# Kernel optimization log

Measured on AMD Instinct MI355X. Metric: run time of the kernel, lower is better.

Reference implementation:

```python
import jax, jax.numpy as jnp
import numpy as np

B, S, HID = 2, 2048, 1024
NUM_HEADS, HEAD_DIM = 16, 64
GRID_SIZE = 16                 # crop_size // patch_size
ROT_DIM = 2 * (HEAD_DIM // 3 // 2)  # = 20, per axial segment (d, h, w)


def setup_inputs() -> dict:
    key = jax.random.key(0)
    ks = jax.random.split(key, 9)
    sc = 1.0 / np.sqrt(HID)
    return {
        "hidden_states": jax.random.normal(ks[0], (B, S, HID), jnp.float32),
        "Wq": jax.random.normal(ks[1], (HID, HID), jnp.float32) * sc,
        "bq": jax.random.normal(ks[2], (HID,), jnp.float32) * 0.02,
        "Wk": jax.random.normal(ks[3], (HID, HID), jnp.float32) * sc,
        "bk": jax.random.normal(ks[4], (HID,), jnp.float32) * 0.02,
        "Wv": jax.random.normal(ks[5], (HID, HID), jnp.float32) * sc,
        "bv": jax.random.normal(ks[6], (HID,), jnp.float32) * 0.02,
        "Wo": jax.random.normal(ks[7], (HID, HID), jnp.float32) * sc,
        "bo": jax.random.normal(ks[8], (HID,), jnp.float32) * 0.02,
    }


def _rotate(x, pos):
    # x: [B, H, S, D], pos: [S] int. Matches torch rotate_queries_or_keys:
    # sin/cos are TILED (repeat) along the last dim, not interleaved.
    D = x.shape[-1]
    half = D // 2
    omega = 1.0 / (10000.0 ** (jnp.arange(half, dtype=x.dtype) / half))
    freq = pos.astype(x.dtype)[:, None] * omega           # [S, half]
    sin = jnp.tile(jnp.sin(freq), (1, 2))                 # [S, D]
    cos = jnp.tile(jnp.cos(freq), (1, 2))
    y = x.reshape(x.shape[:-1] + (half, 2))
    rot = jnp.stack((-y[..., 1], y[..., 0]), axis=-1).reshape(x.shape)
    return x * cos + rot * sin


def _apply_axial_rope(qk, frame_ids, height_ids, width_ids):
    d = ROT_DIM
    parts = [
        _rotate(qk[..., 0:d], frame_ids),
        _rotate(qk[..., d:2 * d], height_ids),
        _rotate(qk[..., 2 * d:3 * d], width_ids),
    ]
    if 3 * d < qk.shape[-1]:
        parts.append(qk[..., 3 * d:])  # un-rotated tail
    return jnp.concatenate(parts, axis=-1)


def reference(hidden_states, Wq, bq, Wk, bk, Wv, bv, Wo, bo):
    Bq, Sq, _ = hidden_states.shape

    def heads(x):  # [B,S,HID] -> [B,H,S,Dh]
        return x.reshape(Bq, Sq, NUM_HEADS, HEAD_DIM).transpose(0, 2, 1, 3)

    q = heads(hidden_states @ Wq + bq)
    k = heads(hidden_states @ Wk + bk)
    v = heads(hidden_states @ Wv + bv)

    # 3D axial position ids from flat token index
    ids = jnp.arange(Sq)
    tokens_per_frame = GRID_SIZE * GRID_SIZE
    frame_ids = ids // tokens_per_frame
    rem = ids - tokens_per_frame * frame_ids
    height_ids = rem // GRID_SIZE
    width_ids = rem - GRID_SIZE * height_ids

    k = _apply_axial_rope(k, frame_ids, height_ids, width_ids)
    q = _apply_axial_rope(q, frame_ids, height_ids, width_ids)

    scaling = HEAD_DIM ** -0.5
    scores = jnp.einsum("bhqd,bhkd->bhqk", q, k) * scaling
    probs = jax.nn.softmax(scores.astype(jnp.float32), axis=-1).astype(q.dtype)
    ctx = jnp.einsum("bhqk,bhkd->bhqd", probs, v)
    ctx = ctx.transpose(0, 2, 1, 3).reshape(Bq, Sq, HID)
    return ctx @ Wo + bo
```

## Files before the change

### kernel.cpp

```cpp
#include <hip/hip_runtime.h>
#include <hip/hip_bf16.h>

#define B_   2
#define S_   2048
#define HID_ 1024
#define NH_  16
#define HD_  64

typedef __hip_bfloat16 bf16;
typedef __attribute__((ext_vector_type(8))) short s8v;
typedef __attribute__((ext_vector_type(4))) float f4v;

#define QSCALE 0.18033688011112042f

__device__ __forceinline__ unsigned short f2b_rne(float x) {
    unsigned int u = __float_as_uint(x);
    u += 0x7fffu + ((u >> 16) & 1u);
    return (unsigned short)(u >> 16);
}

__device__ __forceinline__ void gload_lds16(const void* g, void* l) {
    __builtin_amdgcn_global_load_lds(
        (const __attribute__((address_space(1))) void*)g,
        (__attribute__((address_space(3))) void*)l, 16, 0, 0);
}

__global__ __launch_bounds__(256) void convert_x_kernel(
    const float* __restrict__ X, unsigned short* __restrict__ Xb)
{
    const int i = (blockIdx.x * 256 + threadIdx.x) * 4;
    const float4 f = *reinterpret_cast<const float4*>(X + i);
    ushort4 u;
    u.x = f2b_rne(f.x); u.y = f2b_rne(f.y); u.z = f2b_rne(f.z); u.w = f2b_rne(f.w);
    *reinterpret_cast<ushort4*>(Xb + i) = u;
}

__global__ __launch_bounds__(256) void transpose_w_kernel(
    const float* __restrict__ W0, const float* __restrict__ W1,
    const float* __restrict__ W2, const float* __restrict__ W3,
    unsigned short* __restrict__ T0, unsigned short* __restrict__ T1,
    unsigned short* __restrict__ T2, unsigned short* __restrict__ T3)
{
    const int z = blockIdx.z;
    const float* __restrict__ W = (z == 0) ? W0 : (z == 1) ? W1 : (z == 2) ? W2 : W3;
    unsigned short* __restrict__ T = (z == 0) ? T0 : (z == 1) ? T1 : (z == 2) ? T2 : T3;

    __shared__ float Tl[64][65];
    const int n0 = blockIdx.x * 64, k0 = blockIdx.y * 64;
    const int t = threadIdx.x;
    const int rr = t >> 4, c4 = (t & 15) * 4;

    #pragma unroll
    for (int i = 0; i < 4; ++i) {
        const int kr = i * 16 + rr;
        const float4 f = *reinterpret_cast<const float4*>(W + (size_t)(k0 + kr) * HID_ + n0 + c4);
        Tl[c4 + 0][kr] = f.x; Tl[c4 + 1][kr] = f.y;
        Tl[c4 + 2][kr] = f.z; Tl[c4 + 3][kr] = f.w;
    }
    __syncthreads();
    #pragma unroll
    for (int i = 0; i < 4; ++i) {
        const int nr = i * 16 + rr;
        ushort4 u;
        u.x = f2b_rne(Tl[nr][c4 + 0]); u.y = f2b_rne(Tl[nr][c4 + 1]);
        u.z = f2b_rne(Tl[nr][c4 + 2]); u.w = f2b_rne(Tl[nr][c4 + 3]);
        *reinterpret_cast<ushort4*>(T + (size_t)(n0 + nr) * HID_ + k0 + c4) = u;
    }
}

__device__ __forceinline__ void mfma_mainloop(
    const unsigned short* __restrict__ Ag, const unsigned short* __restrict__ Bg,
    unsigned short* As, unsigned short* Bs,
    int m0, int n0, int t, f4v acc[4][4])
{
    const int w = t >> 6, lane = t & 63;
    const int l15 = lane & 15, qd = lane >> 4;
    const int wm = (w & 1) * 64, wn = (w >> 1) * 64;
    const int srow = w * 8 + (lane >> 3);
    const int lc8  = (((lane & 7) ^ (lane >> 3)) * 8);

    for (int k0 = 0; k0 < HID_; k0 += 64) {
        __syncthreads();
        #pragma unroll
        for (int it = 0; it < 4; ++it) {
            const int row = it * 32 + srow;
            const int sb = (it * 256 + w * 64) * 8;
            gload_lds16(Ag + (size_t)(m0 + row) * HID_ + k0 + lc8, As + sb);
            gload_lds16(Bg + (size_t)(n0 + row) * HID_ + k0 + lc8, Bs + sb);
        }
        __syncthreads();
        #pragma unroll
        for (int kc = 0; kc < 2; ++kc) {
            const int p = ((kc * 4 + qd) ^ (l15 & 7)) * 8;
            s8v af[4], bf[4];
            #pragma unroll
            for (int mt = 0; mt < 4; ++mt)
                af[mt] = *reinterpret_cast<const s8v*>(As + (wm + mt * 16 + l15) * 64 + p);
            #pragma unroll
            for (int nt = 0; nt < 4; ++nt)
                bf[nt] = *reinterpret_cast<const s8v*>(Bs + (wn + nt * 16 + l15) * 64 + p);
            #pragma unroll
            for (int mt = 0; mt < 4; ++mt)
                #pragma unroll
                for (int nt = 0; nt < 4; ++nt)
                    acc[mt][nt] = __builtin_amdgcn_mfma_f32_16x16x32_bf16(
                        af[mt], bf[nt], acc[mt][nt], 0, 0, 0);
        }
    }
}

__global__ __launch_bounds__(256) void gemm_qkv_kernel(
    const unsigned short* __restrict__ Xb,
    const unsigned short* __restrict__ Wqt, const unsigned short* __restrict__ Wkt,
    const unsigned short* __restrict__ Wvt,
    const float* __restrict__ bq, const float* __restrict__ bk, const float* __restrict__ bv,
    unsigned short* __restrict__ Qb, unsigned short* __restrict__ Kb,
    unsigned short* __restrict__ Vt)
{
    const int z = blockIdx.z;
    const unsigned short* __restrict__ Bt = (z == 0) ? Wqt : (z == 1) ? Wkt : Wvt;
    const float* __restrict__ bias = (z == 0) ? bq : (z == 1) ? bk : bv;

    const int n0 = blockIdx.x * 128, m0 = blockIdx.y * 128;
    const int t = threadIdx.x;
    const int w = t >> 6, lane = t & 63;
    const int l15 = lane & 15, qd = lane >> 4;
    const int wm = (w & 1) * 64, wn = (w >> 1) * 64;

    __shared__ unsigned short As[128 * 64];
    __shared__ unsigned short Bs[128 * 64];

    f4v acc[4][4];
    #pragma unroll
    for (int mt = 0; mt < 4; ++mt)
        #pragma unroll
        for (int nt = 0; nt < 4; ++nt) acc[mt][nt] = (f4v){0.f, 0.f, 0.f, 0.f};

    mfma_mainloop(Xb, Bt, As, Bs, m0, n0, t, acc);

    const float osc = (z == 0) ? QSCALE : 1.f;

    #pragma unroll
    for (int nt = 0; nt < 4; ++nt) {
        const int col = n0 + wn + nt * 16 + l15;
        const int h = col >> 6, d = col & 63;
        const float bsc = bias[col];
        const int seg = d / 20;
        const int ds  = d - seg * 20;
        const float om   = __expf(-0.9210340372f * (float)(ds % 10));
        const float sign = (d & 1) ? 1.f : -1.f;

        #pragma unroll
        for (int mt = 0; mt < 4; ++mt) {
            const int mbase = m0 + wm + mt * 16 + qd * 4;
            const int b = mbase >> 11;
            const int sbase = mbase & 2047;
            if (z == 2) {
                ushort4 u;
                unsigned short* up = (unsigned short*)&u;
                #pragma unroll
                for (int r = 0; r < 4; ++r) up[r] = f2b_rne(acc[mt][nt][r] + bsc);
                *reinterpret_cast<ushort4*>(
                    Vt + ((size_t)(b * NH_ + h) * HD_ + d) * S_ + sbase) = u;
            } else {
                unsigned short* __restrict__ dst = (z == 0 ? Qb : Kb)
                    + ((size_t)(b * NH_ + h) * S_ + sbase) * HD_ + d;
                #pragma unroll
                for (int r = 0; r < 4; ++r) {
                    const int s = sbase + r;
                    float v = acc[mt][nt][r] + bsc;
                    const float xp = __shfl_xor(v, 1);
                    if (d < 60) {
                        const int rem = s & 255;
                        const float pos = (float)(seg == 0 ? (s >> 8)
                                               : (seg == 1 ? (rem >> 4) : (rem & 15)));
                        const float a = pos * om;
                        float sn, cs;
                        __sincosf(a, &sn, &cs);
                        v = v * cs + sign * xp * sn;
                    }
                    dst[(size_t)r * HD_] = f2b_rne(v * osc);
                }
            }
        }
    }
}

__global__ __launch_bounds__(256) void gemm_out_kernel(
    const unsigned short* __restrict__ Cb, const unsigned short* __restrict__ Wot,
    const float* __restrict__ bo, float* __restrict__ out)
{
    const int n0 = blockIdx.x * 128, m0 = blockIdx.y * 128;
    const int t = threadIdx.x;
    const int w = t >> 6, lane = t & 63;
    const int l15 = lane & 15, qd = lane >> 4;
    const int wm = (w & 1) * 64, wn = (w >> 1) * 64;

    __shared__ unsigned short As[128 * 64];
    __shared__ unsigned short Bs[128 * 64];

    f4v acc[4][4];
    #pragma unroll
    for (int mt = 0; mt < 4; ++mt)
        #pragma unroll
        for (int nt = 0; nt < 4; ++nt) acc[mt][nt] = (f4v){0.f, 0.f, 0.f, 0.f};

    mfma_mainloop(Cb, Wot, As, Bs, m0, n0, t, acc);

    #pragma unroll
    for (int nt = 0; nt < 4; ++nt) {
        const int col = n0 + wn + nt * 16 + l15;
        const float bsc = bo[col];
        #pragma unroll
        for (int mt = 0; mt < 4; ++mt) {
            const int mbase = m0 + wm + mt * 16 + qd * 4;
            #pragma unroll
            for (int r = 0; r < 4; ++r)
                out[(size_t)(mbase + r) * HID_ + col] = acc[mt][nt][r] + bsc;
        }
    }
}

__global__ __launch_bounds__(256, 2) void attn_kernel(
    const bf16* __restrict__ Qb, const bf16* __restrict__ Kb,
    const bf16* __restrict__ Vt, unsigned short* __restrict__ CTX)
{
    const int q0 = blockIdx.x * 128;
    const int bh = blockIdx.y;
    const int b  = bh >> 4, h = bh & 15;
    const int t  = threadIdx.x;
    const int w  = t >> 6;
    const int lane = t & 63;
    const int l15 = lane & 15, qd = lane >> 4;

    __shared__ unsigned short Ks[128 * 64];
    __shared__ unsigned short Vs[64 * 128];
    __shared__ unsigned short Ps[128 * 136];

    s8v bq[2][2];
    #pragma unroll
    for (int g = 0; g < 2; ++g) {
        const bf16* Qrow = Qb + ((size_t)bh * S_ + q0 + w * 32 + g * 16 + l15) * HD_ + qd * 8;
        bq[g][0] = *reinterpret_cast<const s8v*>(Qrow);
        bq[g][1] = *reinterpret_cast<const s8v*>(Qrow + 32);
    }

    f4v oacc[2][4];
    float lacc[2] = {0.f, 0.f};
    #pragma unroll
    for (int g = 0; g < 2; ++g)
        #pragma unroll
        for (int dt = 0; dt < 4; ++dt) oacc[g][dt] = (f4v){0.f, 0.f, 0.f, 0.f};

    const bf16* __restrict__ Kg = Kb + (size_t)bh * S_ * HD_;
    const bf16* __restrict__ Vg = Vt + (size_t)bh * HD_ * S_;

    const int krow = lane >> 3;
    const int ksw  = ((lane & 7) ^ krow) * 8;
    const int vrow = lane >> 4;

    for (int k0 = 0; k0 < S_; k0 += 128) {
        __syncthreads();
        #pragma unroll
        for (int it = 0; it < 4; ++it) {
            gload_lds16(Kg + (size_t)(k0 + w * 32 + it * 8 + krow) * HD_ + ksw,
                        Ks + (w * 32 + it * 8) * 64);
        }
        #pragma unroll
        for (int it = 0; it < 4; ++it) {
            const int r = w * 16 + it * 4 + vrow;
            const int sv = ((lane & 15) ^ (r & 15)) * 8;
            gload_lds16(Vg + (size_t)r * S_ + k0 + sv,
                        Vs + (w * 16 + it * 4) * 128);
        }
        __syncthreads();

        #pragma unroll
        for (int nt = 0; nt < 8; ++nt) {
            const unsigned short* kr = Ks + (nt * 16 + l15) * 64;
            const s8v ak0 = *reinterpret_cast<const s8v*>(kr + ((qd ^ (l15 & 7)) * 8));
            const s8v ak1 = *reinterpret_cast<const s8v*>(kr + (((qd + 4) ^ (l15 & 7)) * 8));
            #pragma unroll
            for (int g = 0; g < 2; ++g) {
                f4v zz = (f4v){0.f, 0.f, 0.f, 0.f};
                zz = __builtin_amdgcn_mfma_f32_16x16x32_bf16(ak0, bq[g][0], zz, 0, 0, 0);
                zz = __builtin_amdgcn_mfma_f32_16x16x32_bf16(ak1, bq[g][1], zz, 0, 0, 0);
                const float p0 = __builtin_amdgcn_exp2f(zz[0]);
                const float p1 = __builtin_amdgcn_exp2f(zz[1]);
                const float p2 = __builtin_amdgcn_exp2f(zz[2]);
                const float p3 = __builtin_amdgcn_exp2f(zz[3]);
                const unsigned int u01 = __builtin_amdgcn_perm(
                    __float_as_uint(p1), __float_as_uint(p0), 0x07060302u);
                const unsigned int u23 = __builtin_amdgcn_perm(
                    __float_as_uint(p3), __float_as_uint(p2), 0x07060302u);
                const float t0 = __uint_as_float(u01 << 16);
                const float t1 = __uint_as_float(u01 & 0xffff0000u);
                const float t2 = __uint_as_float(u23 << 16);
                const float t3 = __uint_as_float(u23 & 0xffff0000u);
                lacc[g] += (t0 + t1) + (t2 + t3);
                *reinterpret_cast<uint2*>(
                    Ps + (w * 32 + g * 16 + l15) * 136 + nt * 16 + qd * 4) =
                    make_uint2(u01, u23);
            }
        }

        #pragma unroll
        for (int kc = 0; kc < 4; ++kc) {
            s8v ap[2];
            #pragma unroll
            for (int g = 0; g < 2; ++g)
                ap[g] = *reinterpret_cast<const s8v*>(
                    Ps + (w * 32 + g * 16 + l15) * 136 + kc * 32 + qd * 8);
            #pragma unroll
            for (int dt = 0; dt < 4; ++dt) {
                const s8v bv = *reinterpret_cast<const s8v*>(
                    Vs + (dt * 16 + l15) * 128 + (((kc * 4 + qd) ^ l15) & 15) * 8);
                oacc[0][dt] = __builtin_amdgcn_mfma_f32_16x16x32_bf16(ap[0], bv, oacc[0][dt], 0, 0, 0);
                oacc[1][dt] = __builtin_amdgcn_mfma_f32_16x16x32_bf16(ap[1], bv, oacc[1][dt], 0, 0, 0);
            }
        }
    }

    #pragma unroll
    for (int g = 0; g < 2; ++g) {
        float ls = lacc[g];
        ls += __shfl_xor(ls, 16);
        ls += __shfl_xor(ls, 32);
        #pragma unroll
        for (int r = 0; r < 4; ++r) {
            const float lr = __shfl(ls, qd * 4 + r);
            const float inv = 1.0f / lr;
            const int s = q0 + w * 32 + g * 16 + qd * 4 + r;
            unsigned short* __restrict__ dst =
                CTX + ((size_t)(b * S_ + s)) * HID_ + h * HD_ + l15;
            #pragma unroll
            for (int dt = 0; dt < 4; ++dt)
                dst[dt * 16] = f2b_rne(oacc[g][dt][r] * inv);
        }
    }
}

extern "C" void kernel_launch(void* const* d_in, const int* in_sizes, int n_in,
                              void* d_out, int out_size, void* d_ws, size_t ws_size,
                              hipStream_t stream)
{
    const float* X  = (const float*)d_in[0];
    const float* Wq = (const float*)d_in[1];
    const float* bq = (const float*)d_in[2];
    const float* Wk = (const float*)d_in[3];
    const float* bk = (const float*)d_in[4];
    const float* Wv = (const float*)d_in[5];
    const float* bv = (const float*)d_in[6];
    const float* Wo = (const float*)d_in[7];
    const float* bo = (const float*)d_in[8];
    float* out = (float*)d_out;

    const size_t QKV = (size_t)B_ * NH_ * S_ * HD_;
    unsigned short* Xb  = (unsigned short*)d_ws;
    unsigned short* Wqt = Xb  + QKV;
    unsigned short* Wkt = Wqt + (size_t)HID_ * HID_;
    unsigned short* Wvt = Wkt + (size_t)HID_ * HID_;
    unsigned short* Wot = Wvt + (size_t)HID_ * HID_;
    unsigned short* Qb  = Wot + (size_t)HID_ * HID_;
    unsigned short* Kb  = Qb + QKV;
    unsigned short* Vt  = Kb + QKV;
    unsigned short* Cb  = Vt + QKV;

    convert_x_kernel<<<4096, 256, 0, stream>>>(X, Xb);
    transpose_w_kernel<<<dim3(16, 16, 4), 256, 0, stream>>>(
        Wq, Wk, Wv, Wo, Wqt, Wkt, Wvt, Wot);
    gemm_qkv_kernel<<<dim3(8, 32, 3), 256, 0, stream>>>(
        Xb, Wqt, Wkt, Wvt, bq, bk, bv, Qb, Kb, Vt);
    attn_kernel<<<dim3(S_ / 128, B_ * NH_), 256, 0, stream>>>(
        (const bf16*)Qb, (const bf16*)Kb, (const bf16*)Vt, Cb);
    gemm_out_kernel<<<dim3(8, 32), 256, 0, stream>>>(Cb, Wot, bo, out);
}
```

Baseline: 208.3 us.

## Split attention KV range across two blocks, combine partials, fuse prep kernels

Attention now splits the key dimension in half across a new grid z dimension. Each half writes an unnormalized bf16 partial output and its row sums, and a new combine kernel adds the partials and normalizes. The P buffer in LDS shrinks by processing 64 keys at a time, and launch bounds move to 3 blocks per CU, both aimed at more occupancy and parallelism. The X conversion and weight transpose are merged into one prep kernel, and workspace buffers are reused. In exchange there is an extra kernel launch, extra global traffic for the partials, and extra bf16 rounding of the unnormalized partial outputs.

```diff
diff --git a/kernel.cpp b/kernel.cpp
--- a/kernel.cpp
+++ b/kernel.cpp
@@ -19,35 +19,45 @@
     return (unsigned short)(u >> 16);
 }
 
+__device__ __forceinline__ float b2f(unsigned short u) {
+    return __uint_as_float(((unsigned int)u) << 16);
+}
+
 __device__ __forceinline__ void gload_lds16(const void* g, void* l) {
     __builtin_amdgcn_global_load_lds(
         (const __attribute__((address_space(1))) void*)g,
         (__attribute__((address_space(3))) void*)l, 16, 0, 0);
 }
 
-__global__ __launch_bounds__(256) void convert_x_kernel(
-    const float* __restrict__ X, unsigned short* __restrict__ Xb)
-{
-    const int i = (blockIdx.x * 256 + threadIdx.x) * 4;
-    const float4 f = *reinterpret_cast<const float4*>(X + i);
-    ushort4 u;
-    u.x = f2b_rne(f.x); u.y = f2b_rne(f.y); u.z = f2b_rne(f.z); u.w = f2b_rne(f.w);
-    *reinterpret_cast<ushort4*>(Xb + i) = u;
-}
-
-__global__ __launch_bounds__(256) void transpose_w_kernel(
+__global__ __launch_bounds__(256) void prep_kernel(
+    const float* __restrict__ X,
     const float* __restrict__ W0, const float* __restrict__ W1,
     const float* __restrict__ W2, const float* __restrict__ W3,
+    unsigned short* __restrict__ Xb,
     unsigned short* __restrict__ T0, unsigned short* __restrict__ T1,
     unsigned short* __restrict__ T2, unsigned short* __restrict__ T3)
 {
     const int z = blockIdx.z;
+    const int t = threadIdx.x;
+
+    if (z >= 4) {
+        const size_t base = ((size_t)(z - 4) * 256 + blockIdx.y * 16 + blockIdx.x) * 4096;
+        #pragma unroll
+        for (int p = 0; p < 4; ++p) {
+            const size_t i = base + p * 1024 + t * 4;
+            const float4 f = *reinterpret_cast<const float4*>(X + i);
+            ushort4 u;
+            u.x = f2b_rne(f.x); u.y = f2b_rne(f.y); u.z = f2b_rne(f.z); u.w = f2b_rne(f.w);
+            *reinterpret_cast<ushort4*>(Xb + i) = u;
+        }
+        return;
+    }
+
     const float* __restrict__ W = (z == 0) ? W0 : (z == 1) ? W1 : (z == 2) ? W2 : W3;
     unsigned short* __restrict__ T = (z == 0) ? T0 : (z == 1) ? T1 : (z == 2) ? T2 : T3;
 
     __shared__ float Tl[64][65];
     const int n0 = blockIdx.x * 64, k0 = blockIdx.y * 64;
-    const int t = threadIdx.x;
     const int rr = t >> 4, c4 = (t & 15) * 4;
 
     #pragma unroll
@@ -221,12 +231,15 @@
     }
 }
 
-__global__ __launch_bounds__(256, 2) void attn_kernel(
+__global__ __launch_bounds__(256, 3) void attn_kernel(
     const bf16* __restrict__ Qb, const bf16* __restrict__ Kb,
-    const bf16* __restrict__ Vt, unsigned short* __restrict__ CTX)
+    const bf16* __restrict__ Vt,
+    unsigned short* __restrict__ O0, unsigned short* __restrict__ O1,
+    float* __restrict__ Lp)
 {
     const int q0 = blockIdx.x * 128;
     const int bh = blockIdx.y;
+    const int half = blockIdx.z;
     const int b  = bh >> 4, h = bh & 15;
     const int t  = threadIdx.x;
     const int w  = t >> 6;
@@ -235,7 +248,7 @@
 
     __shared__ unsigned short Ks[128 * 64];
     __shared__ unsigned short Vs[64 * 128];
-    __shared__ unsigned short Ps[128 * 136];
+    __shared__ unsigned short Ps[128 * 72];
 
     s8v bq[2][2];
     #pragma unroll
@@ -259,7 +272,8 @@
     const int ksw  = ((lane & 7) ^ krow) * 8;
     const int vrow = lane >> 4;
 
-    for (int k0 = 0; k0 < S_; k0 += 128) {
+    const int kbeg = half * 1024;
+    for (int k0 = kbeg; k0 < kbeg + 1024; k0 += 128) {
         __syncthreads();
         #pragma unroll
         for (int it = 0; it < 4; ++it) {
@@ -276,68 +290,103 @@
         __syncthreads();
 
         #pragma unroll
-        for (int nt = 0; nt < 8; ++nt) {
-            const unsigned short* kr = Ks + (nt * 16 + l15) * 64;
-            const s8v ak0 = *reinterpret_cast<const s8v*>(kr + ((qd ^ (l15 & 7)) * 8));
-            const s8v ak1 = *reinterpret_cast<const s8v*>(kr + (((qd + 4) ^ (l15 & 7)) * 8));
-            #pragma unroll
-            for (int g = 0; g < 2; ++g) {
-                f4v zz = (f4v){0.f, 0.f, 0.f, 0.f};
-                zz = __builtin_amdgcn_mfma_f32_16x16x32_bf16(ak0, bq[g][0], zz, 0, 0, 0);
-                zz = __builtin_amdgcn_mfma_f32_16x16x32_bf16(ak1, bq[g][1], zz, 0, 0, 0);
-                const float p0 = __builtin_amdgcn_exp2f(zz[0]);
-                const float p1 = __builtin_amdgcn_exp2f(zz[1]);
-                const float p2 = __builtin_amdgcn_exp2f(zz[2]);
-                const float p3 = __builtin_amdgcn_exp2f(zz[3]);
-                const unsigned int u01 = __builtin_amdgcn_perm(
-                    __float_as_uint(p1), __float_as_uint(p0), 0x07060302u);
-                const unsigned int u23 = __builtin_amdgcn_perm(
-                    __float_as_uint(p3), __float_as_uint(p2), 0x07060302u);
-                const float t0 = __uint_as_float(u01 << 16);
-                const float t1 = __uint_as_float(u01 & 0xffff0000u);
-                const float t2 = __uint_as_float(u23 << 16);
-                const float t3 = __uint_as_float(u23 & 0xffff0000u);
-                lacc[g] += (t0 + t1) + (t2 + t3);
-                *reinterpret_cast<uint2*>(
-                    Ps + (w * 32 + g * 16 + l15) * 136 + nt * 16 + qd * 4) =
-                    make_uint2(u01, u23);
+        for (int hi = 0; hi < 2; ++hi) {
+            #pragma unroll
+            for (int nth = 0; nth < 4; ++nth) {
+                const unsigned short* kr = Ks + (hi * 64 + nth * 16 + l15) * 64;
+                const s8v ak0 = *reinterpret_cast<const s8v*>(kr + ((qd ^ (l15 & 7)) * 8));
+                const s8v ak1 = *reinterpret_cast<const s8v*>(kr + (((qd + 4) ^ (l15 & 7)) * 8));
+                #pragma unroll
+                for (int g = 0; g < 2; ++g) {
+                    f4v zz = (f4v){0.f, 0.f, 0.f, 0.f};
+                    zz = __builtin_amdgcn_mfma_f32_16x16x32_bf16(ak0, bq[g][0], zz, 0, 0, 0);
+                    zz = __builtin_amdgcn_mfma_f32_16x16x32_bf16(ak1, bq[g][1], zz, 0, 0, 0);
+                    const float p0 = __builtin_amdgcn_exp2f(zz[0]);
+                    const float p1 = __builtin_amdgcn_exp2f(zz[1]);
+                    const float p2 = __builtin_amdgcn_exp2f(zz[2]);
+                    const float p3 = __builtin_amdgcn_exp2f(zz[3]);
+                    const unsigned int u01 = __builtin_amdgcn_perm(
+                        __float_as_uint(p1), __float_as_uint(p0), 0x07060302u);
+                    const unsigned int u23 = __builtin_amdgcn_perm(
+                        __float_as_uint(p3), __float_as_uint(p2), 0x07060302u);
+                    const float t0 = __uint_as_float(u01 << 16);
+                    const float t1 = __uint_as_float(u01 & 0xffff0000u);
+                    const float t2 = __uint_as_float(u23 << 16);
+                    const float t3 = __uint_as_float(u23 & 0xffff0000u);
+                    lacc[g] += (t0 + t1) + (t2 + t3);
+                    *reinterpret_cast<uint2*>(
+                        Ps + (w * 32 + g * 16 + l15) * 72 + nth * 16 + qd * 4) =
+                        make_uint2(u01, u23);
+                }
             }
-        }
-
-        #pragma unroll
-        for (int kc = 0; kc < 4; ++kc) {
-            s8v ap[2];
-            #pragma unroll
-            for (int g = 0; g < 2; ++g)
-                ap[g] = *reinterpret_cast<const s8v*>(
-                    Ps + (w * 32 + g * 16 + l15) * 136 + kc * 32 + qd * 8);
-            #pragma unroll
-            for (int dt = 0; dt < 4; ++dt) {
-                const s8v bv = *reinterpret_cast<const s8v*>(
-                    Vs + (dt * 16 + l15) * 128 + (((kc * 4 + qd) ^ l15) & 15) * 8);
-                oacc[0][dt] = __builtin_amdgcn_mfma_f32_16x16x32_bf16(ap[0], bv, oacc[0][dt], 0, 0, 0);
-                oacc[1][dt] = __builtin_amdgcn_mfma_f32_16x16x32_bf16(ap[1], bv, oacc[1][dt], 0, 0, 0);
+
+            #pragma unroll
+            for (int kcl = 0; kcl < 2; ++kcl) {
+                const int kc = hi * 2 + kcl;
+                s8v ap[2];
+                #pragma unroll
+                for (int g = 0; g < 2; ++g)
+                    ap[g] = *reinterpret_cast<const s8v*>(
+                        Ps + (w * 32 + g * 16 + l15) * 72 + kcl * 32 + qd * 8);
+                #pragma unroll
+                for (int dt = 0; dt < 4; ++dt) {
+                    const s8v bv = *reinterpret_cast<const s8v*>(
+                        Vs + (dt * 16 + l15) * 128 + (((kc * 4 + qd) ^ l15) & 15) * 8);
+                    oacc[0][dt] = __builtin_amdgcn_mfma_f32_16x16x32_bf16(ap[0], bv, oacc[0][dt], 0, 0, 0);
+                    oacc[1][dt] = __builtin_amdgcn_mfma_f32_16x16x32_bf16(ap[1], bv, oacc[1][dt], 0, 0, 0);
+                }
             }
         }
     }
 
+    unsigned short* __restrict__ Oh = half ? O1 : O0;
     #pragma unroll
     for (int g = 0; g < 2; ++g) {
         float ls = lacc[g];
         ls += __shfl_xor(ls, 16);
         ls += __shfl_xor(ls, 32);
+        if (qd == 0)
+            Lp[((size_t)(half * 32 + bh)) * S_ + q0 + w * 32 + g * 16 + l15] = ls;
         #pragma unroll
         for (int r = 0; r < 4; ++r) {
-            const float lr = __shfl(ls, qd * 4 + r);
-            const float inv = 1.0f / lr;
             const int s = q0 + w * 32 + g * 16 + qd * 4 + r;
             unsigned short* __restrict__ dst =
-                CTX + ((size_t)(b * S_ + s)) * HID_ + h * HD_ + l15;
+                Oh + ((size_t)(b * S_ + s)) * HID_ + h * HD_ + l15;
             #pragma unroll
             for (int dt = 0; dt < 4; ++dt)
-                dst[dt * 16] = f2b_rne(oacc[g][dt][r] * inv);
-        }
-    }
+                dst[dt * 16] = f2b_rne(oacc[g][dt][r]);
+        }
+    }
+}
+
+__global__ __launch_bounds__(256) void combine_kernel(
+    const unsigned short* __restrict__ O0, const unsigned short* __restrict__ O1,
+    const float* __restrict__ Lp, unsigned short* __restrict__ Cb)
+{
+    const size_t e = ((size_t)blockIdx.x * 256 + threadIdx.x) * 8;
+    const int hid = (int)(e & 1023);
+    const int s   = (int)((e >> 10) & 2047);
+    const int b   = (int)(e >> 21);
+    const int bh  = b * NH_ + (hid >> 6);
+    const float L0 = Lp[(size_t)bh * S_ + s];
+    const float L1 = Lp[(size_t)(32 + bh) * S_ + s];
+    const float inv = 1.0f / (L0 + L1);
+
+    const ushort4 a0 = *reinterpret_cast<const ushort4*>(O0 + e);
+    const ushort4 a1 = *reinterpret_cast<const ushort4*>(O0 + e + 4);
+    const ushort4 c0 = *reinterpret_cast<const ushort4*>(O1 + e);
+    const ushort4 c1 = *reinterpret_cast<const ushort4*>(O1 + e + 4);
+    ushort4 r0, r1;
+    r0.x = f2b_rne((b2f(a0.x) + b2f(c0.x)) * inv);
+    r0.y = f2b_rne((b2f(a0.y) + b2f(c0.y)) * inv);
+    r0.z = f2b_rne((b2f(a0.z) + b2f(c0.z)) * inv);
+    r0.w = f2b_rne((b2f(a0.w) + b2f(c0.w)) * inv);
+    r1.x = f2b_rne((b2f(a1.x) + b2f(c1.x)) * inv);
+    r1.y = f2b_rne((b2f(a1.y) + b2f(c1.y)) * inv);
+    r1.z = f2b_rne((b2f(a1.z) + b2f(c1.z)) * inv);
+    r1.w = f2b_rne((b2f(a1.w) + b2f(c1.w)) * inv);
+    *reinterpret_cast<ushort4*>(Cb + e) = r0;
+    *reinterpret_cast<ushort4*>(Cb + e + 4) = r1;
 }
 
 extern "C" void kernel_launch(void* const* d_in, const int* in_sizes, int n_in,
@@ -356,22 +405,26 @@
     float* out = (float*)d_out;
 
     const size_t QKV = (size_t)B_ * NH_ * S_ * HD_;
-    unsigned short* Xb  = (unsigned short*)d_ws;
+    const size_t WSZ = (size_t)HID_ * HID_;
+    unsigned short* Wot = (unsigned short*)d_ws;
+    unsigned short* Xb  = Wot + WSZ;
     unsigned short* Wqt = Xb  + QKV;
-    unsigned short* Wkt = Wqt + (size_t)HID_ * HID_;
-    unsigned short* Wvt = Wkt + (size_t)HID_ * HID_;
-    unsigned short* Wot = Wvt + (size_t)HID_ * HID_;
-    unsigned short* Qb  = Wot + (size_t)HID_ * HID_;
+    unsigned short* Wkt = Wqt + WSZ;
+    unsigned short* Wvt = Wkt + WSZ;
+    unsigned short* Qb  = Wvt + WSZ;
     unsigned short* Kb  = Qb + QKV;
     unsigned short* Vt  = Kb + QKV;
     unsigned short* Cb  = Vt + QKV;
-
-    convert_x_kernel<<<4096, 256, 0, stream>>>(X, Xb);
-    transpose_w_kernel<<<dim3(16, 16, 4), 256, 0, stream>>>(
-        Wq, Wk, Wv, Wo, Wqt, Wkt, Wvt, Wot);
+    unsigned short* O1  = Cb + QKV;
+    unsigned short* O0  = Xb;
+    float*          Lp  = (float*)Wqt;
+
+    prep_kernel<<<dim3(16, 16, 8), 256, 0, stream>>>(
+        X, Wq, Wk, Wv, Wo, Xb, Wqt, Wkt, Wvt, Wot);
     gemm_qkv_kernel<<<dim3(8, 32, 3), 256, 0, stream>>>(
         Xb, Wqt, Wkt, Wvt, bq, bk, bv, Qb, Kb, Vt);
-    attn_kernel<<<dim3(S_ / 128, B_ * NH_), 256, 0, stream>>>(
-        (const bf16*)Qb, (const bf16*)Kb, (const bf16*)Vt, Cb);
+    attn_kernel<<<dim3(S_ / 128, B_ * NH_, 2), 256, 0, stream>>>(
+        (const bf16*)Qb, (const bf16*)Kb, (const bf16*)Vt, O0, O1, Lp);
+    combine_kernel<<<2048, 256, 0, stream>>>(O0, O1, Lp, Cb);
     gemm_out_kernel<<<dim3(8, 32), 256, 0, stream>>>(Cb, Wot, bo, out);
 }
```

Result: slower. 216.2 us (+3.8%).
